# Optimization experiments

Hardware: AMD Instinct MI355X
Metric: run time of the kernel (lower is better)

The kernel has to match this reference:

```python
import jax, jax.numpy as jnp
import numpy as np

DIM = 1024
B, K = 8192, 16


def setup_inputs() -> dict:
    key = jax.random.key(0)
    ks = jax.random.split(key, 7)
    # xavier_uniform bound for square [C,C]: sqrt(6/(C+C))
    bq = float(np.sqrt(6.0 / (DIM + DIM)))
    ba_bound = float(np.sqrt(6.0 / (DIM + 1)))
    return {
        "query": jax.random.normal(ks[0], (B, DIM), dtype=jnp.float32),
        "key": jax.random.normal(ks[1], (B, K, DIM), dtype=jnp.float32),
        "value": jax.random.normal(ks[2], (B, K, DIM), dtype=jnp.float32),
        "Wq": jax.random.uniform(ks[3], (DIM, DIM), jnp.float32, -bq, bq),
        "Wk": jax.random.uniform(ks[4], (DIM, DIM), jnp.float32, -bq, bq),
        "Wa": jax.random.uniform(ks[5], (1, DIM), jnp.float32, -ba_bound, ba_bound),
        "ba": jnp.ones((1,), dtype=jnp.float32),
    }


def reference(query, key, value, Wq, Wk, Wa, ba):
    # query: [B, C]; key/value: [B, K, C]
    C = query.shape[-1]
    res = query
    q = query[:, None, :]                       # [B, 1, C]
    k = jnp.concatenate([q, key], axis=1)       # [B, K+1, C] (query prepended)
    v = jnp.concatenate([q, value], axis=1)     # [B, K+1, C]
    qp = q @ Wq.T                               # [B, 1, C]
    kp = k @ Wk.T                               # [B, K+1, C]
    scale = 1.0 / jnp.sqrt(jnp.asarray(C, dtype=jnp.float32))
    scores = jnp.einsum('bqc,bkc->bqk', qp, kp) * scale   # [B, 1, K+1]
    attn_w = jax.nn.softmax(scores, axis=-1)
    attn = jnp.einsum('bqk,bkc->bqc', attn_w, v)[:, 0, :]  # [B, C]
    alpha = jax.nn.sigmoid(res @ Wa.T + ba)     # [B, 1]
    out = res + alpha * attn                    # gated residual
    # F.normalize(p=2, dim=-1, eps=1e-12)
    norm = jnp.linalg.norm(out, axis=-1, keepdims=True)
    return out / jnp.maximum(norm, 1e-12)
```

## Files before the change

### kernel.cpp

```cpp
#include <hip/hip_runtime.h>
#include <hip/hip_bf16.h>

#define DIM   1024
#define BATCH 8192
#define KV    16

typedef __attribute__((ext_vector_type(4))) float f32x4;
typedef __attribute__((ext_vector_type(8))) short short8;

static __device__ __forceinline__ unsigned short f2bf(float x) {
  return __builtin_bit_cast(unsigned short, __float2bfloat16(x));
}
static __device__ __forceinline__ float bf2f(unsigned short x) {
  return __bfloat162float(__builtin_bit_cast(__hip_bfloat16, x));
}
static __device__ __forceinline__ float dot4(f32x4 a, f32x4 b) {
  return a.x * b.x + a.y * b.y + a.z * b.z + a.w * b.w;
}

static __device__ __forceinline__ void gl_lds16(const unsigned short* g, unsigned short* l) {
  __builtin_amdgcn_global_load_lds(
      (const __attribute__((address_space(1))) void*)g,
      (__attribute__((address_space(3))) void*)l, 16, 0, 0);
}

__global__ __launch_bounds__(256) void transpose_w(const float* __restrict__ Wq,
                                                   const float* __restrict__ Wk,
                                                   unsigned short* __restrict__ WqT,
                                                   unsigned short* __restrict__ WkT) {
  __shared__ float tile[32][33];
  const float* src = blockIdx.z ? Wk : Wq;
  unsigned short* dst = blockIdx.z ? WkT : WqT;
  int tx = threadIdx.x & 31, ty = threadIdx.x >> 5;
  int x = blockIdx.x * 32 + tx;
  int y0 = blockIdx.y * 32;
  #pragma unroll
  for (int i = ty; i < 32; i += 8)
    tile[i][tx] = src[(size_t)(y0 + i) * DIM + x];
  __syncthreads();
  int x2 = blockIdx.y * 32 + tx;
  int y2 = blockIdx.x * 32;
  #pragma unroll
  for (int i = ty; i < 32; i += 8)
    dst[(size_t)(y2 + i) * DIM + x2] = f2bf(tile[tx][i]);
}

__global__ __launch_bounds__(256) void gemm_nt64(const unsigned short* __restrict__ A,
                                                 const unsigned short* __restrict__ B,
                                                 unsigned short* __restrict__ C,
                                                 int N, int K) {
  __shared__ __align__(16) unsigned short As[64 * 32];
  __shared__ __align__(16) unsigned short Bs[64 * 32];
  const int tid = threadIdx.x;
  const int lane = tid & 63;
  const int wave = tid >> 6;
  const int wr = wave >> 1, wc = wave & 1;
  const size_t bm = (size_t)blockIdx.x * 64;
  const size_t bn = (size_t)blockIdx.y * 64;

  f32x4 acc[2][2];
  #pragma unroll
  for (int m = 0; m < 2; ++m)
    #pragma unroll
    for (int n = 0; n < 2; ++n)
      acc[m][n] = (f32x4){0.f, 0.f, 0.f, 0.f};

  const int r0 = tid >> 2;
  const int cc = (tid & 3) * 8;
  const int kg = lane >> 4;
  const int rowf = lane & 15;

  for (int kt = 0; kt < K; kt += 32) {
    gl_lds16(A + (bm + r0) * K + kt + cc, As + tid * 8);
    gl_lds16(B + (bn + r0) * K + kt + cc, Bs + tid * 8);
    __syncthreads();
    short8 af[2], bfr[2];
    #pragma unroll
    for (int m = 0; m < 2; ++m)
      af[m] = *(const short8*)(As + ((wr * 32 + m * 16 + rowf) * 32 + kg * 8));
    #pragma unroll
    for (int n = 0; n < 2; ++n)
      bfr[n] = *(const short8*)(Bs + ((wc * 32 + n * 16 + rowf) * 32 + kg * 8));
    #pragma unroll
    for (int m = 0; m < 2; ++m)
      #pragma unroll
      for (int n = 0; n < 2; ++n)
        acc[m][n] = __builtin_amdgcn_mfma_f32_16x16x32_bf16(af[m], bfr[n], acc[m][n], 0, 0, 0);
    __syncthreads();
  }

  const int rq = (lane >> 4) * 4;
  const int colf = lane & 15;
  #pragma unroll
  for (int m = 0; m < 2; ++m)
    #pragma unroll
    for (int n = 0; n < 2; ++n)
      #pragma unroll
      for (int i = 0; i < 4; ++i)
        C[(bm + wr * 32 + m * 16 + rq + i) * N + bn + wc * 32 + n * 16 + colf] =
            f2bf(acc[m][n][i]);
}

__global__ __launch_bounds__(256) void gemm_u(const float* __restrict__ Af,
                                              const unsigned short* __restrict__ B,
                                              unsigned short* __restrict__ C,
                                              int ntN, int ldc) {
  __shared__ __align__(16) unsigned short As[128 * 32];
  __shared__ __align__(16) unsigned short Bs[128 * 32];

  const int cpx = gridDim.x >> 3;
  const int wg = (blockIdx.x & 7) * cpx + (blockIdx.x >> 3);
  const size_t bm = (size_t)(wg / ntN) * 128;
  const size_t bn = (size_t)(wg % ntN) * 128;

  const int tid = threadIdx.x;
  const int lane = tid & 63;
  const int wave = tid >> 6;
  const int wr = wave >> 1, wc = wave & 1;

  f32x4 acc[4][4];
  #pragma unroll
  for (int m = 0; m < 4; ++m)
    #pragma unroll
    for (int n = 0; n < 4; ++n)
      acc[m][n] = (f32x4){0.f, 0.f, 0.f, 0.f};

  const int kg = lane >> 4;
  const int rowf = lane & 15;
  const int br0 = tid >> 2;
  const int bcc = (tid & 3) * 8;

  for (int kt = 0; kt < DIM; kt += 32) {
    gl_lds16(B + (bn + br0) * DIM + kt + bcc, Bs + tid * 8);
    gl_lds16(B + (bn + 64 + br0) * DIM + kt + bcc, Bs + 2048 + tid * 8);
    #pragma unroll
    for (int it = 0; it < 4; ++it) {
      int c = it * 256 + tid;
      int r = c >> 3;
      int ko = (c & 7) * 4;
      f32x4 f = *(const f32x4*)(Af + (bm + r) * DIM + kt + ko);
      ushort4 o;
      o.x = f2bf(f.x); o.y = f2bf(f.y); o.z = f2bf(f.z); o.w = f2bf(f.w);
      *(ushort4*)(As + r * 32 + ko) = o;
    }
    __syncthreads();
    short8 af[4], bfr[4];
    #pragma unroll
    for (int m = 0; m < 4; ++m)
      af[m] = *(const short8*)(As + ((wr * 64 + m * 16 + rowf) * 32 + kg * 8));
    #pragma unroll
    for (int n = 0; n < 4; ++n)
      bfr[n] = *(const short8*)(Bs + ((wc * 64 + n * 16 + rowf) * 32 + kg * 8));
    #pragma unroll
    for (int m = 0; m < 4; ++m)
      #pragma unroll
      for (int n = 0; n < 4; ++n)
        acc[m][n] = __builtin_amdgcn_mfma_f32_16x16x32_bf16(af[m], bfr[n], acc[m][n], 0, 0, 0);
    __syncthreads();
  }

  const int rq = (lane >> 4) * 4;
  const int colf = lane & 15;
  #pragma unroll
  for (int m = 0; m < 4; ++m)
    #pragma unroll
    for (int n = 0; n < 4; ++n)
      #pragma unroll
      for (int i = 0; i < 4; ++i) {
        size_t row = bm + wr * 64 + m * 16 + rq + i;
        size_t col = bn + wc * 64 + n * 16 + colf;
        C[row * (size_t)ldc + col] = f2bf(acc[m][n][i]);
      }
}

__global__ __launch_bounds__(256) void epilogue(const float* __restrict__ query,
                                                const float* __restrict__ key,
                                                const float* __restrict__ value,
                                                const float* __restrict__ Wa,
                                                const float* __restrict__ ba,
                                                const unsigned short* __restrict__ u,
                                                float* __restrict__ out) {
  const int b = blockIdx.x;
  const int tid = threadIdx.x;
  const int lane = tid & 63, wave = tid >> 6;
  const f32x4* k4 = (const f32x4*)(key + (size_t)b * KV * DIM);
  const f32x4* v4 = (const f32x4*)(value + (size_t)b * KV * DIM);

  f32x4 qv = ((const f32x4*)(query + (size_t)b * DIM))[tid];
  ushort4 ub = ((const ushort4*)(u + (size_t)b * 2048))[tid];
  f32x4 uv;
  uv.x = bf2f(ub.x); uv.y = bf2f(ub.y); uv.z = bf2f(ub.z); uv.w = bf2f(ub.w);
  f32x4 wv = ((const f32x4*)Wa)[tid];

  float s[17];
  s[0] = dot4(qv, uv);
  float ad = dot4(qv, wv);
  #pragma unroll
  for (int j = 1; j <= 16; ++j) {
    f32x4 kv = __builtin_nontemporal_load(k4 + (j - 1) * 256 + tid);
    s[j] = dot4(uv, kv);
  }

  f32x4 vv[16];
  #pragma unroll
  for (int j = 0; j < 16; ++j)
    vv[j] = __builtin_nontemporal_load(v4 + j * 256 + tid);

  #pragma unroll
  for (int m = 32; m >= 1; m >>= 1) {
    #pragma unroll
    for (int j = 0; j < 17; ++j) s[j] += __shfl_xor(s[j], m);
    ad += __shfl_xor(ad, m);
  }
  __shared__ float red[4][18];
  if (lane == 0) {
    #pragma unroll
    for (int j = 0; j < 17; ++j) red[wave][j] = s[j];
    red[wave][17] = ad;
  }
  __syncthreads();

  float wt[17];
  float mx = -1e30f;
  #pragma unroll
  for (int j = 0; j < 17; ++j) {
    float t = (red[0][j] + red[1][j] + red[2][j] + red[3][j]) * 0.03125f;
    wt[j] = t;
    mx = fmaxf(mx, t);
  }
  float den = 0.f;
  #pragma unroll
  for (int j = 0; j < 17; ++j) {
    wt[j] = expf(wt[j] - mx);
    den += wt[j];
  }
  float adt = red[0][17] + red[1][17] + red[2][17] + red[3][17] + ba[0];
  float alpha = 1.0f / (1.0f + expf(-adt));
  float am = alpha / den;

  f32x4 acc = qv * wt[0];
  #pragma unroll
  for (int j = 1; j <= 16; ++j) acc += vv[j - 1] * wt[j];
  f32x4 t = qv + acc * am;

  float ssp = dot4(t, t);
  #pragma unroll
  for (int m = 32; m >= 1; m >>= 1) ssp += __shfl_xor(ssp, m);
  __shared__ float red2[4];
  if (lane == 0) red2[wave] = ssp;
  __syncthreads();
  float nrm = sqrtf(red2[0] + red2[1] + red2[2] + red2[3]);
  float inv = 1.0f / fmaxf(nrm, 1e-12f);

  __builtin_nontemporal_store(t * inv, (f32x4*)(out + (size_t)b * DIM) + tid);
}

extern "C" void kernel_launch(void* const* d_in, const int* in_sizes, int n_in,
                              void* d_out, int out_size, void* d_ws, size_t ws_size,
                              hipStream_t stream) {
  const float* query = (const float*)d_in[0];
  const float* key   = (const float*)d_in[1];
  const float* value = (const float*)d_in[2];
  const float* Wq    = (const float*)d_in[3];
  const float* Wk    = (const float*)d_in[4];
  const float* Wa    = (const float*)d_in[5];
  const float* ba    = (const float*)d_in[6];

  unsigned short* WqT = (unsigned short*)d_ws;
  unsigned short* WkT = WqT + (size_t)DIM * DIM;
  unsigned short* Mt  = WkT + (size_t)DIM * DIM;
  unsigned short* ubf = (unsigned short*)d_out;

  transpose_w<<<dim3(32, 32, 2), 256, 0, stream>>>(Wq, Wk, WqT, WkT);
  gemm_nt64<<<dim3(16, 16), 256, 0, stream>>>(WkT, WqT, Mt, DIM, DIM);
  gemm_u<<<512, 256, 0, stream>>>(query, Mt, ubf, DIM / 128, 2048);
  epilogue<<<BATCH, 256, 0, stream>>>(query, key, value, Wa, ba, ubf, (float*)d_out);
}
```

Measured before the change: 244.3 us.

## Fuse weight transpose and bf16 conversion into the Wk^T·Wq product GEMM

Drops the separate transpose_w kernel. The small GEMM now reads fp32 Wq and Wk directly, converts them to bf16, and writes them transposed into LDS. This saves one kernel launch and the bf16 workspace round trip, at the cost of scattered 2-byte LDS stores that may bank-conflict. The epilogue also issues the value loads before the key loads to start memory traffic earlier.

```diff
diff --git a/kernel.cpp b/kernel.cpp
--- a/kernel.cpp
+++ b/kernel.cpp
@@ -24,31 +24,9 @@
       (__attribute__((address_space(3))) void*)l, 16, 0, 0);
 }
 
-__global__ __launch_bounds__(256) void transpose_w(const float* __restrict__ Wq,
-                                                   const float* __restrict__ Wk,
-                                                   unsigned short* __restrict__ WqT,
-                                                   unsigned short* __restrict__ WkT) {
-  __shared__ float tile[32][33];
-  const float* src = blockIdx.z ? Wk : Wq;
-  unsigned short* dst = blockIdx.z ? WkT : WqT;
-  int tx = threadIdx.x & 31, ty = threadIdx.x >> 5;
-  int x = blockIdx.x * 32 + tx;
-  int y0 = blockIdx.y * 32;
-  #pragma unroll
-  for (int i = ty; i < 32; i += 8)
-    tile[i][tx] = src[(size_t)(y0 + i) * DIM + x];
-  __syncthreads();
-  int x2 = blockIdx.y * 32 + tx;
-  int y2 = blockIdx.x * 32;
-  #pragma unroll
-  for (int i = ty; i < 32; i += 8)
-    dst[(size_t)(y2 + i) * DIM + x2] = f2bf(tile[tx][i]);
-}
-
-__global__ __launch_bounds__(256) void gemm_nt64(const unsigned short* __restrict__ A,
-                                                 const unsigned short* __restrict__ B,
-                                                 unsigned short* __restrict__ C,
-                                                 int N, int K) {
+__global__ __launch_bounds__(256) void mt_fused(const float* __restrict__ Wq,
+                                                const float* __restrict__ Wk,
+                                                unsigned short* __restrict__ Mt) {
   __shared__ __align__(16) unsigned short As[64 * 32];
   __shared__ __align__(16) unsigned short Bs[64 * 32];
   const int tid = threadIdx.x;
@@ -65,14 +43,25 @@
     for (int n = 0; n < 2; ++n)
       acc[m][n] = (f32x4){0.f, 0.f, 0.f, 0.f};
 
-  const int r0 = tid >> 2;
-  const int cc = (tid & 3) * 8;
+  const int cloc = tid >> 3;
+  const int e8 = (tid & 7) * 8;
   const int kg = lane >> 4;
   const int rowf = lane & 15;
 
-  for (int kt = 0; kt < K; kt += 32) {
-    gl_lds16(A + (bm + r0) * K + kt + cc, As + tid * 8);
-    gl_lds16(B + (bn + r0) * K + kt + cc, Bs + tid * 8);
+  for (int kt = 0; kt < DIM; kt += 32) {
+    const size_t c = kt + cloc;
+    f32x4 a0 = *(const f32x4*)(Wk + c * DIM + bm + e8);
+    f32x4 a1 = *(const f32x4*)(Wk + c * DIM + bm + e8 + 4);
+    f32x4 b0 = *(const f32x4*)(Wq + c * DIM + bn + e8);
+    f32x4 b1 = *(const f32x4*)(Wq + c * DIM + bn + e8 + 4);
+    As[(e8 + 0) * 32 + cloc] = f2bf(a0.x); As[(e8 + 1) * 32 + cloc] = f2bf(a0.y);
+    As[(e8 + 2) * 32 + cloc] = f2bf(a0.z); As[(e8 + 3) * 32 + cloc] = f2bf(a0.w);
+    As[(e8 + 4) * 32 + cloc] = f2bf(a1.x); As[(e8 + 5) * 32 + cloc] = f2bf(a1.y);
+    As[(e8 + 6) * 32 + cloc] = f2bf(a1.z); As[(e8 + 7) * 32 + cloc] = f2bf(a1.w);
+    Bs[(e8 + 0) * 32 + cloc] = f2bf(b0.x); Bs[(e8 + 1) * 32 + cloc] = f2bf(b0.y);
+    Bs[(e8 + 2) * 32 + cloc] = f2bf(b0.z); Bs[(e8 + 3) * 32 + cloc] = f2bf(b0.w);
+    Bs[(e8 + 4) * 32 + cloc] = f2bf(b1.x); Bs[(e8 + 5) * 32 + cloc] = f2bf(b1.y);
+    Bs[(e8 + 6) * 32 + cloc] = f2bf(b1.z); Bs[(e8 + 7) * 32 + cloc] = f2bf(b1.w);
     __syncthreads();
     short8 af[2], bfr[2];
     #pragma unroll
@@ -97,7 +86,7 @@
     for (int n = 0; n < 2; ++n)
       #pragma unroll
       for (int i = 0; i < 4; ++i)
-        C[(bm + wr * 32 + m * 16 + rq + i) * N + bn + wc * 32 + n * 16 + colf] =
+        Mt[(bm + wr * 32 + m * 16 + rq + i) * DIM + bn + wc * 32 + n * 16 + colf] =
             f2bf(acc[m][n][i]);
 }
 
@@ -192,6 +181,11 @@
   uv.x = bf2f(ub.x); uv.y = bf2f(ub.y); uv.z = bf2f(ub.z); uv.w = bf2f(ub.w);
   f32x4 wv = ((const f32x4*)Wa)[tid];
 
+  f32x4 vv[16];
+  #pragma unroll
+  for (int j = 0; j < 16; ++j)
+    vv[j] = __builtin_nontemporal_load(v4 + j * 256 + tid);
+
   float s[17];
   s[0] = dot4(qv, uv);
   float ad = dot4(qv, wv);
@@ -200,11 +194,6 @@
     f32x4 kv = __builtin_nontemporal_load(k4 + (j - 1) * 256 + tid);
     s[j] = dot4(uv, kv);
   }
-
-  f32x4 vv[16];
-  #pragma unroll
-  for (int j = 0; j < 16; ++j)
-    vv[j] = __builtin_nontemporal_load(v4 + j * 256 + tid);
 
   #pragma unroll
   for (int m = 32; m >= 1; m >>= 1) {
@@ -266,13 +255,10 @@
   const float* Wa    = (const float*)d_in[5];
   const float* ba    = (const float*)d_in[6];
 
-  unsigned short* WqT = (unsigned short*)d_ws;
-  unsigned short* WkT = WqT + (size_t)DIM * DIM;
-  unsigned short* Mt  = WkT + (size_t)DIM * DIM;
+  unsigned short* Mt  = (unsigned short*)d_ws;
   unsigned short* ubf = (unsigned short*)d_out;
 
-  transpose_w<<<dim3(32, 32, 2), 256, 0, stream>>>(Wq, Wk, WqT, WkT);
-  gemm_nt64<<<dim3(16, 16), 256, 0, stream>>>(WkT, WqT, Mt, DIM, DIM);
+  mt_fused<<<dim3(16, 16), 256, 0, stream>>>(Wq, Wk, Mt);
   gemm_u<<<512, 256, 0, stream>>>(query, Mt, ubf, DIM / 128, 2048);
   epilogue<<<BATCH, 256, 0, stream>>>(query, key, value, Wa, ba, ubf, (float*)d_out);
 }
```

Measured after the change: 257.5 us. +5.4%, slower.
